# Kernel tuning notes

Hardware: AMD Instinct MI355X
Metric: run time of the kernel (lower is better)

The kernel has to match this reference:

```python
import jax, jax.numpy as jnp
import numpy as np

QC = 12          # effective quantum channels (quantum_channels//4*4)
G = 3            # number of 4-channel quantum groups
DIM = 128
NGROUPS_GN = 8
NUM_LAYER = 1

# PauliZ sign table: wire 0 is the most-significant qubit (PennyLane default.qubit)
_SIGNS = np.array([[1.0 - 2.0 * ((k >> (3 - w)) & 1) for w in range(4)]
                   for k in range(16)], dtype=np.float32)


def _apply_rx(state, phi, w):
    # state: [B,2,2,2,2] complex64; phi: [B]; RX = cos(p/2) I - i sin(p/2) X
    c = jnp.cos(0.5 * phi).astype(jnp.complex64)
    s = (-1j) * jnp.sin(0.5 * phi).astype(jnp.complex64)
    U = jnp.stack([jnp.stack([c, s], -1), jnp.stack([s, c], -1)], -2)  # [B,2,2]
    st = jnp.moveaxis(state, 1 + w, -1)
    st = jnp.einsum('bij,b...j->b...i', U, st)
    return jnp.moveaxis(st, -1, 1 + w)


def _apply_cnot(state, c, t):
    st = jnp.moveaxis(state, (1 + c, 1 + t), (-2, -1))
    st = jnp.concatenate([st[..., 0:1, :], st[..., 1:2, ::-1]], axis=-2)
    return jnp.moveaxis(st, (-2, -1), (1 + c, 1 + t))


def _circuit(x4, theta):
    # AngleEmbedding(RX) + NUM_LAYER x Basic_ansatz; x4: [B,4], theta: [4*NUM_LAYER]
    B = x4.shape[0]
    state = jnp.zeros((B, 2, 2, 2, 2), jnp.complex64).at[:, 0, 0, 0, 0].set(1.0)
    for w in range(4):
        state = _apply_rx(state, x4[:, w], w)
    for l in range(NUM_LAYER):
        th = theta[4 * l:4 * (l + 1)]
        for w in range(4):
            state = _apply_rx(state, jnp.broadcast_to(th[w], (B,)), w)
        for c in range(3):
            state = _apply_cnot(state, c, c + 1)
        state = _apply_cnot(state, 3, 0)
    probs = jnp.abs(state.reshape(B, 16)) ** 2
    return probs @ jnp.asarray(_SIGNS)  # [B,4] PauliZ expvals


def _quantum_block(x_q, qparams):
    # x_q: [B,H,W,QC]; pool spatially, run per-group circuit, broadcast back
    B, H, W, Cq = x_q.shape
    pooled = jnp.mean(x_q, axis=(1, 2)).reshape(B, Cq // 4, 4)
    y = jax.vmap(_circuit, in_axes=(1, 0), out_axes=1)(pooled, qparams)  # [B,G,4]
    y = y.reshape(B, 1, 1, Cq)
    return jnp.broadcast_to(y, (B, H, W, Cq))


def _ws_conv(x, kernel, bias):
    eps = 1e-5  # fp32 branch of WeightStandardizedConv
    mean = jnp.mean(kernel, axis=(0, 1, 2), keepdims=True)
    var = jnp.var(kernel, axis=(0, 1, 2), keepdims=True)
    k = (kernel - mean) / jnp.sqrt(var + eps)
    y = jax.lax.conv_general_dilated(x, k, (1, 1), ((1, 1), (1, 1)),
                                     dimension_numbers=('NHWC', 'HWIO', 'NHWC'))
    return y + bias


def _group_norm(x, scale, bias, groups=NGROUPS_GN, eps=1e-6):
    B, H, W, C = x.shape
    xg = x.reshape(B, H, W, groups, C // groups)
    mu = jnp.mean(xg, axis=(1, 2, 4), keepdims=True)
    var = jnp.var(xg, axis=(1, 2, 4), keepdims=True)
    xn = ((xg - mu) / jnp.sqrt(var + eps)).reshape(B, H, W, C)
    return xn * scale + bias


def setup_inputs() -> dict:
    key = jax.random.key(0)
    ks = jax.random.split(key, 8)
    B, H, W, C, T = 16, 64, 64, DIM, 512
    cc = DIM - QC  # classical conv channels = 116
    return {
        'x': jax.random.normal(ks[0], (B, H, W, C), jnp.float32),
        'time_emb': jax.random.normal(ks[1], (B, T), jnp.float32),
        'qparams': jax.random.uniform(ks[2], (G, 4), jnp.float32),
        'conv0_kernel': jax.random.normal(ks[3], (3, 3, cc, cc), jnp.float32) * 0.05,
        'conv0_bias': jnp.zeros((cc,), jnp.float32),
        'conv1_kernel': jax.random.normal(ks[4], (3, 3, cc, cc), jnp.float32) * 0.05,
        'conv1_bias': jnp.zeros((cc,), jnp.float32),
        'gn0_scale': jnp.ones((C,), jnp.float32),
        'gn0_bias': jnp.zeros((C,), jnp.float32),
        'gn1_scale': jnp.ones((C,), jnp.float32),
        'gn1_bias': jnp.zeros((C,), jnp.float32),
        'time_w': jax.random.normal(ks[5], (T, 2 * DIM), jnp.float32) * 0.02,
        'time_b': jnp.zeros((2 * DIM,), jnp.float32),
    }


def reference(x, time_emb, qparams, conv0_kernel, conv0_bias, conv1_kernel,
              conv1_bias, gn0_scale, gn0_bias, gn1_scale, gn1_bias, time_w, time_b):
    # first quantum + classical branch
    h_q = _quantum_block(x[..., :QC], qparams)
    h_c = _ws_conv(x[..., QC:], conv0_kernel, conv0_bias)
    h = jnp.concatenate([h_q, h_c], axis=-1)
    h = _group_norm(h, gn0_scale, gn0_bias)
    # FiLM conditioning from time embedding
    t = jax.nn.swish(time_emb) @ time_w + time_b  # [B, 2*DIM]
    scale, shift = jnp.split(t[:, None, None, :], 2, axis=-1)
    h = jax.nn.swish(h * (1 + scale) + shift)
    # second quantum + classical branch
    h_q2 = _quantum_block(h[..., :QC], qparams)
    h_c2 = _ws_conv(h[..., QC:], conv1_kernel, conv1_bias)
    h2 = jnp.concatenate([h_q2, h_c2], axis=-1)
    h2 = jax.nn.swish(_group_norm(h2, gn1_scale, gn1_bias))
    return x + h2
```

## Files before the change

kernel.cpp:

```cpp
#include <hip/hip_runtime.h>
#include <math.h>

#define BATCH 16
#define NPX 4096
#define CDIM 128
#define CC 116
#define KTAPS 1044

using u16 = unsigned short;
typedef __attribute__((ext_vector_type(8))) short short8;
typedef __attribute__((ext_vector_type(16))) float f32x16;

__device__ __forceinline__ float swishf(float z) {
    return z / (1.f + __expf(-z));
}
__device__ __forceinline__ float bf2f(u16 u) {
    union { unsigned int i; float f; } v; v.i = ((unsigned int)u) << 16; return v.f;
}
__device__ __forceinline__ u16 f2bf(float f) {
    union { float f; unsigned int i; } v; v.f = f;
    unsigned int r = v.i + 0x7fffu + ((v.i >> 16) & 1u);
    return (u16)(r >> 16);
}

__global__ void k_init(float* __restrict__ p) {
    int i = blockIdx.x * 256 + threadIdx.x;
    if (i < 8384) p[i] = 0.f;
}

__global__ void k_pool(const float* __restrict__ x, float* __restrict__ pooled) {
    int b = blockIdx.x;
    int tid = threadIdx.x;
    float s[12];
#pragma unroll
    for (int c = 0; c < 12; ++c) s[c] = 0.f;
    const float* xb = x + (size_t)b * NPX * CDIM;
    for (int px = tid; px < NPX; px += 256) {
        const float4* p = (const float4*)(xb + (size_t)px * CDIM);
        float4 v0 = p[0], v1 = p[1], v2 = p[2];
        s[0] += v0.x; s[1] += v0.y; s[2] += v0.z; s[3] += v0.w;
        s[4] += v1.x; s[5] += v1.y; s[6] += v1.z; s[7] += v1.w;
        s[8] += v2.x; s[9] += v2.y; s[10] += v2.z; s[11] += v2.w;
    }
    __shared__ float red[12][256];
#pragma unroll
    for (int c = 0; c < 12; ++c) red[c][tid] = s[c];
    __syncthreads();
    for (int st = 128; st > 0; st >>= 1) {
        if (tid < st) {
#pragma unroll
            for (int c = 0; c < 12; ++c) red[c][tid] += red[c][tid + st];
        }
        __syncthreads();
    }
    if (tid < 12) pooled[b * 12 + tid] = red[tid][0] * (1.f / 4096.f);
}

__device__ void run_circuit(const float* ang, const float* th, float* z) {
    float ar[16], ai[16];
#pragma unroll
    for (int k = 0; k < 16; ++k) { ar[k] = 0.f; ai[k] = 0.f; }
    ar[0] = 1.f;
#pragma unroll
    for (int pass = 0; pass < 2; ++pass) {
        const float* a = pass ? th : ang;
#pragma unroll
        for (int w = 0; w < 4; ++w) {
            float half = 0.5f * a[w];
            float cth = cosf(half), sth = sinf(half);
            int m = 1 << (3 - w);
#pragma unroll
            for (int k = 0; k < 16; ++k) {
                if (k & m) continue;
                int k2 = k | m;
                float r0 = ar[k], i0 = ai[k], r1 = ar[k2], i1 = ai[k2];
                ar[k]  = cth * r0 + sth * i1;
                ai[k]  = cth * i0 - sth * r1;
                ar[k2] = sth * i0 + cth * r1;
                ai[k2] = -sth * r0 + cth * i1;
            }
        }
    }
#pragma unroll
    for (int e = 0; e < 4; ++e) {
        const int cwi[4] = {0, 1, 2, 3};
        const int twi[4] = {1, 2, 3, 0};
        int mc = 1 << (3 - cwi[e]), mt = 1 << (3 - twi[e]);
#pragma unroll
        for (int k = 0; k < 16; ++k) {
            if ((k & mc) && !(k & mt)) {
                int k2 = k | mt;
                float tr = ar[k]; ar[k] = ar[k2]; ar[k2] = tr;
                float ti = ai[k]; ai[k] = ai[k2]; ai[k2] = ti;
            }
        }
    }
    float zz[4] = {0.f, 0.f, 0.f, 0.f};
#pragma unroll
    for (int k = 0; k < 16; ++k) {
        float p = ar[k] * ar[k] + ai[k] * ai[k];
#pragma unroll
        for (int w = 0; w < 4; ++w) zz[w] += ((k >> (3 - w)) & 1) ? -p : p;
    }
#pragma unroll
    for (int w = 0; w < 4; ++w) z[w] = zz[w];
}

__global__ void k_circ1(const float* __restrict__ pooled, const float* __restrict__ qp,
                        float* __restrict__ y1) {
    int tid = threadIdx.x;
    if (tid >= 48) return;
    int b = tid / 3, g = tid % 3;
    float z[4];
    run_circuit(pooled + b * 12 + g * 4, qp + g * 4, z);
#pragma unroll
    for (int w = 0; w < 4; ++w) y1[b * 12 + g * 4 + w] = z[w];
}

__global__ void k_time(const float* __restrict__ te, const float* __restrict__ W,
                       const float* __restrict__ tb, float* __restrict__ t) {
    int b = blockIdx.x, tid = threadIdx.x;
    __shared__ float se[512];
    for (int k = tid; k < 512; k += 256) {
        float z = te[b * 512 + k];
        se[k] = swishf(z);
    }
    __syncthreads();
    float acc = tb[tid];
    for (int k = 0; k < 512; ++k) acc += se[k] * W[k * 256 + tid];
    t[b * 256 + tid] = acc;
}

__global__ void k_wstd(const float* __restrict__ K0, const float* __restrict__ K1,
                       u16* __restrict__ kqp0, u16* __restrict__ kqp1) {
    const float* K = blockIdx.y ? K1 : K0;
    u16* kqp = blockIdx.y ? kqp1 : kqp0;
    int o = blockIdx.x;
    int tid = threadIdx.x;
    __shared__ float rs[256], rss[256];
    __shared__ float mb[2];
    float s = 0.f, ss = 0.f;
    if (o < CC) {
        for (int idx = tid; idx < KTAPS; idx += 256) {
            float v = K[(size_t)idx * CC + o];
            s += v; ss += v * v;
        }
    }
    rs[tid] = s; rss[tid] = ss;
    __syncthreads();
    for (int st = 128; st > 0; st >>= 1) {
        if (tid < st) { rs[tid] += rs[tid + st]; rss[tid] += rss[tid + st]; }
        __syncthreads();
    }
    if (tid == 0) {
        float m = rs[0] * (1.f / KTAPS);
        float var = rss[0] * (1.f / KTAPS) - m * m;
        mb[0] = m;
        mb[1] = rsqrtf(var + 1e-5f);
    }
    __syncthreads();
    float m = mb[0], inv = mb[1];
    for (int idx = tid; idx < 1152; idx += 256) {
        int tap = idx >> 7, ic = idx & 127;
        float v = 0.f;
        if (o < CC && ic < CC) v = (K[((size_t)tap * CC + ic) * CC + o] - m) * inv;
        int step = tap * 8 + (ic >> 4);
        int lane2 = ((ic >> 3) & 1) * 32 + (o & 31);
        int j = ic & 7;
        kqp[(size_t)(step * 4 + (o >> 5)) * 512 + lane2 * 8 + j] = f2bf(v);
    }
}

template <int MODE>
__launch_bounds__(256)
__global__ void k_conv(const void* __restrict__ inp, const float* __restrict__ Acoef,
                       const float* __restrict__ Bcoef, const u16* __restrict__ kqp,
                       const float* __restrict__ bias, u16* __restrict__ outp,
                       float* __restrict__ csum) {
    __shared__ u16 As[4 * 64 * 128];
    const int hb = blockIdx.x;
    const int hp = ((hb & 7) << 2) | (hb >> 3);
    const int h0 = hp * 2;
    const int b = blockIdx.y;
    const int tid = threadIdx.x, lane = tid & 63, wid = tid >> 6;
    const int wm = wid & 1, wn = wid >> 1;

    const u16* bp = kqp + ((size_t)(wn * 2) << 9) + ((size_t)lane << 3);
    short8 breg[6][2];
#pragma unroll
    for (int s = 0; s < 6; ++s) {
        breg[s][0] = *(const short8*)(bp + ((size_t)s << 11));
        breg[s][1] = *(const short8*)(bp + ((size_t)s << 11) + 512);
    }

    const int pp = tid >> 2, ck = tid & 3;
    const int swz = (pp & 15) << 4;
    char* asb = (char*)As;

    float ca[32], cb[32];
    if (MODE == 1) {
        const float* ap = Acoef + b * 128 + 12 + ck * 32;
        const float* bpc = Bcoef + b * 128 + 12 + ck * 32;
        if (ck < 3) {
#pragma unroll
            for (int j = 0; j < 8; ++j) {
                *(float4*)&ca[j * 4] = ((const float4*)ap)[j];
                *(float4*)&cb[j * 4] = ((const float4*)bpc)[j];
            }
        } else {
#pragma unroll
            for (int j = 0; j < 5; ++j) {
                *(float4*)&ca[j * 4] = ((const float4*)ap)[j];
                *(float4*)&cb[j * 4] = ((const float4*)bpc)[j];
            }
        }
    }

#pragma unroll
    for (int r = 0; r < 4; ++r) {
        const int hi = h0 + r - 1;
        const bool valid = (hi >= 0 && hi < 64);
        u16 t[32];
        if (valid) {
            const size_t px = (size_t)((b * 64 + hi) * 64 + pp);
            if (MODE == 0) {
                const float* s = (const float*)inp + px * 128 + 12 + ck * 32;
                if (ck < 3) {
                    float v[32];
#pragma unroll
                    for (int j = 0; j < 8; ++j) *(float4*)&v[j * 4] = ((const float4*)s)[j];
#pragma unroll
                    for (int e = 0; e < 32; ++e) t[e] = f2bf(v[e]);
                } else {
                    float v[20];
#pragma unroll
                    for (int j = 0; j < 5; ++j) *(float4*)&v[j * 4] = ((const float4*)s)[j];
#pragma unroll
                    for (int e = 0; e < 20; ++e) t[e] = f2bf(v[e]);
#pragma unroll
                    for (int e = 20; e < 32; ++e) t[e] = 0;
                }
            } else {
                const u16* s = (const u16*)inp + px * 128 + ck * 32;
                if (ck < 3) {
                    short8 v[4];
#pragma unroll
                    for (int k = 0; k < 4; ++k) v[k] = ((const short8*)s)[k];
#pragma unroll
                    for (int e = 0; e < 32; ++e) {
                        float f = bf2f((u16)v[e >> 3][e & 7]);
                        t[e] = f2bf(swishf(f * ca[e] + cb[e]));
                    }
                } else {
                    short8 v[3];
#pragma unroll
                    for (int k = 0; k < 3; ++k) v[k] = ((const short8*)s)[k];
#pragma unroll
                    for (int e = 0; e < 20; ++e) {
                        float f = bf2f((u16)v[e >> 3][e & 7]);
                        t[e] = f2bf(swishf(f * ca[e] + cb[e]));
                    }
#pragma unroll
                    for (int e = 20; e < 32; ++e) t[e] = 0;
                }
            }
        } else {
#pragma unroll
            for (int e = 0; e < 32; ++e) t[e] = 0;
        }
        char* rowb = asb + (r * 64 + pp) * 256;
#pragma unroll
        for (int k = 0; k < 4; ++k)
            *(short8*)(rowb + (((ck * 64 + k * 16)) ^ swz)) = *(const short8*)&t[k * 8];
    }

    const int l31 = lane & 31;
    const int chpart = (lane >> 5) << 4;
    int rowoff[3], swzv[3];
#pragma unroll
    for (int q = 0; q < 3; ++q) {
        int ppx = l31 + q - 1;
        int ppc = ppx < 0 ? 0 : ppx;
        rowoff[q] = ppc << 7;
        swzv[q] = (ppc & 15) << 4;
    }
    int rowoff1[3], swzv1[3];
#pragma unroll
    for (int q = 0; q < 3; ++q) {
        int ppx = 32 + l31 + q - 1;
        int ppc = ppx > 63 ? 63 : ppx;
        rowoff1[q] = ppc << 7;
        swzv1[q] = (ppc & 15) << 4;
    }
    const bool edge_lo = (l31 == 0);
    const bool edge_hi = (l31 == 31);
    const short8 zero8 = {0, 0, 0, 0, 0, 0, 0, 0};
    const u16* aw = As + wm * 8192;

    __syncthreads();

    f32x16 acc[2][2];
#pragma unroll
    for (int mf = 0; mf < 2; ++mf)
#pragma unroll
        for (int nf = 0; nf < 2; ++nf)
#pragma unroll
            for (int r = 0; r < 16; ++r) acc[mf][nf][r] = 0.f;

    short8 afrag[2][2];
    afrag[0][0] = *(const short8*)&aw[rowoff[0] + ((chpart ^ swzv[0]) >> 1)];
    afrag[0][1] = *(const short8*)&aw[rowoff1[0] + ((chpart ^ swzv1[0]) >> 1)];

#pragma unroll
    for (int s = 0; s < 72; ++s) {
        const int tap = s >> 3;
        const int p = tap / 3, q = tap % 3;
        const int slotB = s % 6;
        const int cur = s & 1, nxt = cur ^ 1;
        if (s + 1 < 72) {
            const int t2 = (s + 1) >> 3;
            const int p2 = t2 / 3, q2 = t2 % 3;
            const int cb2 = ((s + 1) & 7) << 5;
            afrag[nxt][0] = *(const short8*)&aw[p2 * 8192 + rowoff[q2]
                             + (((cb2 + chpart) ^ swzv[q2]) >> 1)];
            afrag[nxt][1] = *(const short8*)&aw[p2 * 8192 + rowoff1[q2]
                             + (((cb2 + chpart) ^ swzv1[q2]) >> 1)];
        }
        short8 a0 = afrag[cur][0], a1 = afrag[cur][1];
        if (q == 0) a0 = edge_lo ? zero8 : a0;
        if (q == 2) a1 = edge_hi ? zero8 : a1;
        acc[0][0] = __builtin_amdgcn_mfma_f32_32x32x16_bf16(a0, breg[slotB][0], acc[0][0], 0, 0, 0);
        acc[0][1] = __builtin_amdgcn_mfma_f32_32x32x16_bf16(a0, breg[slotB][1], acc[0][1], 0, 0, 0);
        acc[1][0] = __builtin_amdgcn_mfma_f32_32x32x16_bf16(a1, breg[slotB][0], acc[1][0], 0, 0, 0);
        acc[1][1] = __builtin_amdgcn_mfma_f32_32x32x16_bf16(a1, breg[slotB][1], acc[1][1], 0, 0, 0);
        if (s + 6 < 72) {
            breg[slotB][0] = *(const short8*)(bp + ((size_t)(s + 6) << 11));
            breg[slotB][1] = *(const short8*)(bp + ((size_t)(s + 6) << 11) + 512);
        }
    }

    float bv[2], cs[2], cq[2];
#pragma unroll
    for (int nf = 0; nf < 2; ++nf) {
        int oc = wn * 64 + nf * 32 + l31;
        bv[nf] = (oc < CC) ? bias[oc] : 0.f;
        cs[nf] = 0.f; cq[nf] = 0.f;
    }
    const int rbase = (lane >> 5) * 4;
    size_t obase = (size_t)(b * 4096 + (h0 + wm) * 64) * 128;
#pragma unroll
    for (int mf = 0; mf < 2; ++mf)
#pragma unroll
        for (int nf = 0; nf < 2; ++nf) {
            int oc = wn * 64 + nf * 32 + l31;
#pragma unroll
            for (int r = 0; r < 16; ++r) {
                int row = (r & 3) + ((r >> 2) << 3) + rbase;
                int px = mf * 32 + row;
                float v = acc[mf][nf][r] + bv[nf];
                outp[obase + (size_t)px * 128 + oc] = f2bf(v);
                cs[nf] += v;
                cq[nf] += v * v;
            }
        }
#pragma unroll
    for (int nf = 0; nf < 2; ++nf) {
        cs[nf] += __shfl_xor(cs[nf], 32);
        cq[nf] += __shfl_xor(cq[nf], 32);
        if (lane < 32) {
            int oc = wn * 64 + nf * 32 + l31;
            atomicAdd(&csum[(b * 128 + oc) * 2], cs[nf]);
            atomicAdd(&csum[(b * 128 + oc) * 2 + 1], cq[nf]);
        }
    }
}

__global__ void k_mid0(const float* __restrict__ csum, const float* __restrict__ y1,
                       const float* __restrict__ t, const float* __restrict__ gs,
                       const float* __restrict__ gb, const float* __restrict__ qp,
                       float* __restrict__ A, float* __restrict__ Bc,
                       float* __restrict__ y2) {
    __shared__ float sst[128][2];
    int tid = threadIdx.x;
    if (tid < 128) {
        int b = tid >> 3, g = tid & 7;
        float S = 0.f, SS = 0.f;
#pragma unroll
        for (int e = 0; e < 16; ++e) {
            int orig = g * 16 + e;
            if (orig >= 12) {
                int cc = orig - 12;
                S += csum[(b * 128 + cc) * 2];
                SS += csum[(b * 128 + cc) * 2 + 1];
            }
        }
        if (g == 0) {
#pragma unroll
            for (int c = 0; c < 12; ++c) {
                float v = y1[b * 12 + c];
                S += 4096.f * v;
                SS += 4096.f * v * v;
            }
        }
        float mu = S * (1.f / 65536.f);
        float var = SS * (1.f / 65536.f) - mu * mu;
        sst[tid][0] = mu;
        sst[tid][1] = rsqrtf(var + 1e-6f);
    }
    __syncthreads();
    for (int i = tid; i < 2048; i += 256) {
        int b = i >> 7, c = i & 127, g = c >> 4;
        float mu = sst[b * 8 + g][0], isd = sst[b * 8 + g][1];
        float sc = t[b * 256 + c], sh = t[b * 256 + 128 + c];
        float a = isd * gs[c];
        float bb = gb[c] - mu * a;
        A[i] = a * (1.f + sc);
        Bc[i] = bb * (1.f + sc) + sh;
    }
    if (tid < 48) {
        int b = tid / 3, gq = tid % 3;
        float pin[4], z[4];
        float mu = sst[b * 8][0], isd = sst[b * 8][1];
#pragma unroll
        for (int w = 0; w < 4; ++w) {
            int c = gq * 4 + w;
            float a = isd * gs[c];
            float bb = gb[c] - mu * a;
            float sc = t[b * 256 + c], sh = t[b * 256 + 128 + c];
            float v = y1[b * 12 + c];
            pin[w] = swishf(v * (a * (1.f + sc)) + (bb * (1.f + sc) + sh));
        }
        run_circuit(pin, qp + gq * 4, z);
#pragma unroll
        for (int w = 0; w < 4; ++w) y2[b * 12 + gq * 4 + w] = z[w];
    }
}

__global__ void k_mid1(const float* __restrict__ csum, const float* __restrict__ y2,
                       const float* __restrict__ gs, const float* __restrict__ gb,
                       float* __restrict__ A2, float* __restrict__ B2,
                       float* __restrict__ oq) {
    __shared__ float sst[128][2];
    int tid = threadIdx.x;
    if (tid < 128) {
        int b = tid >> 3, g = tid & 7;
        float S = 0.f, SS = 0.f;
#pragma unroll
        for (int e = 0; e < 16; ++e) {
            int orig = g * 16 + e;
            if (orig >= 12) {
                int cc = orig - 12;
                S += csum[(b * 128 + cc) * 2];
                SS += csum[(b * 128 + cc) * 2 + 1];
            }
        }
        if (g == 0) {
#pragma unroll
            for (int c = 0; c < 12; ++c) {
                float v = y2[b * 12 + c];
                S += 4096.f * v;
                SS += 4096.f * v * v;
            }
        }
        float mu = S * (1.f / 65536.f);
        float var = SS * (1.f / 65536.f) - mu * mu;
        sst[tid][0] = mu;
        sst[tid][1] = rsqrtf(var + 1e-6f);
    }
    __syncthreads();
    for (int i = tid; i < 2048; i += 256) {
        int b = i >> 7, c = i & 127, g = c >> 4;
        float mu = sst[b * 8 + g][0], isd = sst[b * 8 + g][1];
        float a = isd * gs[c];
        A2[i] = a;
        B2[i] = gb[c] - mu * a;
    }
    if (tid < 192) {
        int b = tid / 12, c = tid % 12;
        float mu = sst[b * 8][0], isd = sst[b * 8][1];
        float a = isd * gs[c];
        float bb = gb[c] - mu * a;
        oq[b * 12 + c] = swishf(y2[b * 12 + c] * a + bb);
    }
}

__global__ void k_final(const float* __restrict__ x, const u16* __restrict__ co,
                        const float* __restrict__ A2, const float* __restrict__ B2,
                        const float* __restrict__ oq, float* __restrict__ outp) {
    const int t = blockIdx.x, b = blockIdx.y;
    const int seg = t >> 6, hraw = t & 63;
    const int h = ((hraw & 7) << 3) | (hraw >> 3);
    const int tid = threadIdx.x;
    const size_t px = (size_t)(b * 64 + h) * 64 + seg * 8 + (tid >> 5);
    const int c4 = tid & 31, c = c4 * 4;
    float4 xv = *(const float4*)(x + px * CDIM + c);
    float4 r;
    if (c4 < 3) {
        const float* q = oq + b * 12 + c;
        r.x = xv.x + q[0]; r.y = xv.y + q[1]; r.z = xv.z + q[2]; r.w = xv.w + q[3];
    } else {
        int cc = c - 12;
        const u16* hp = co + px * 128 + cc;
        float4 a = *(const float4*)(A2 + b * 128 + c);
        float4 bb = *(const float4*)(B2 + b * 128 + c);
        r.x = xv.x + swishf(bf2f(hp[0]) * a.x + bb.x);
        r.y = xv.y + swishf(bf2f(hp[1]) * a.y + bb.y);
        r.z = xv.z + swishf(bf2f(hp[2]) * a.z + bb.z);
        r.w = xv.w + swishf(bf2f(hp[3]) * a.w + bb.w);
    }
    *(float4*)(outp + px * CDIM + c) = r;
}

extern "C" void kernel_launch(void* const* d_in, const int* in_sizes, int n_in,
                              void* d_out, int out_size, void* d_ws, size_t ws_size,
                              hipStream_t stream) {
    const float* x        = (const float*)d_in[0];
    const float* time_emb = (const float*)d_in[1];
    const float* qparams  = (const float*)d_in[2];
    const float* c0k      = (const float*)d_in[3];
    const float* c0b      = (const float*)d_in[4];
    const float* c1k      = (const float*)d_in[5];
    const float* c1b      = (const float*)d_in[6];
    const float* g0s      = (const float*)d_in[7];
    const float* g0b      = (const float*)d_in[8];
    const float* g1s      = (const float*)d_in[9];
    const float* g1b      = (const float*)d_in[10];
    const float* tw       = (const float*)d_in[11];
    const float* tb       = (const float*)d_in[12];
    float* outp = (float*)d_out;
    float* ws = (float*)d_ws;

    size_t o = 0;
    auto alloc = [&](size_t n) { size_t r = o; o += (n + 15) & ~(size_t)15; return r; };
    float* zbase  = ws + alloc(8384);
    float* pooled = zbase;
    float* csum0  = zbase + 192;
    float* csum1  = zbase + 192 + 4096;
    float* y1     = ws + alloc(192);
    float* y2     = ws + alloc(192);
    float* t      = ws + alloc(4096);
    float* A      = ws + alloc(2048);
    float* Bc     = ws + alloc(2048);
    float* A2     = ws + alloc(2048);
    float* B2     = ws + alloc(2048);
    float* oq     = ws + alloc(192);
    u16* kqp0     = (u16*)(ws + alloc(73728));
    u16* kqp1     = (u16*)(ws + alloc(73728));
    u16* convA    = (u16*)(ws + alloc(4194304));
    u16* convB    = (u16*)(ws + alloc(4194304));

    k_init<<<33, 256, 0, stream>>>(zbase);
    k_pool<<<16, 256, 0, stream>>>(x, pooled);
    k_time<<<16, 256, 0, stream>>>(time_emb, tw, tb, t);
    k_wstd<<<dim3(128, 2), 256, 0, stream>>>(c0k, c1k, kqp0, kqp1);
    k_circ1<<<1, 64, 0, stream>>>(pooled, qparams, y1);

    dim3 cgrid(32, 16);
    k_conv<0><<<cgrid, 256, 0, stream>>>(x, nullptr, nullptr, kqp0, c0b, convA, csum0);
    k_mid0<<<1, 256, 0, stream>>>(csum0, y1, t, g0s, g0b, qparams, A, Bc, y2);

    k_conv<1><<<cgrid, 256, 0, stream>>>(convA, A, Bc, kqp1, c1b, convB, csum1);
    k_mid1<<<1, 256, 0, stream>>>(csum1, y2, g1s, g1b, A2, B2, oq);
    k_final<<<dim3(512, 16), 256, 0, stream>>>(x, convB, A2, B2, oq, outp);
}
```

Measured before the change: 135.9 us.

## Split conv LDS staging to overlap MFMA on first rows with loading the rest

The conv kernel now issues all four input-row global loads up front, writes only rows 0-1 to LDS, and starts MFMA on taps using those rows (the first 24 steps). Rows 2-3 are converted and stored only after that, behind a second barrier. It also uses the hardware packed bf16 convert instruction, raises MFMA priority with s_setprio, shrinks the B-register prefetch ring from 6 to 3 slots, and sets launch_bounds to 2 blocks per SM. Holding the raw rows in registers increases register pressure, and the shallower B prefetch may expose more load latency.

Result: faster. 129.9 us (-4.4%).

```diff
diff --git a/kernel.cpp b/kernel.cpp
--- a/kernel.cpp
+++ b/kernel.cpp
@@ -21,6 +21,11 @@
     union { float f; unsigned int i; } v; v.f = f;
     unsigned int r = v.i + 0x7fffu + ((v.i >> 16) & 1u);
     return (u16)(r >> 16);
+}
+__device__ __forceinline__ unsigned cvtpk(float a, float b) {
+    unsigned r;
+    asm("v_cvt_pk_bf16_f32 %0, %1, %2" : "=v"(r) : "v"(a), "v"(b));
+    return r;
 }
 
 __global__ void k_init(float* __restrict__ p) {
@@ -172,7 +177,7 @@
 }
 
 template <int MODE>
-__launch_bounds__(256)
+__launch_bounds__(256, 2)
 __global__ void k_conv(const void* __restrict__ inp, const float* __restrict__ Acoef,
                        const float* __restrict__ Bcoef, const u16* __restrict__ kqp,
                        const float* __restrict__ bias, u16* __restrict__ outp,
@@ -184,95 +189,85 @@
     const int b = blockIdx.y;
     const int tid = threadIdx.x, lane = tid & 63, wid = tid >> 6;
     const int wm = wid & 1, wn = wid >> 1;
-
-    const u16* bp = kqp + ((size_t)(wn * 2) << 9) + ((size_t)lane << 3);
-    short8 breg[6][2];
-#pragma unroll
-    for (int s = 0; s < 6; ++s) {
-        breg[s][0] = *(const short8*)(bp + ((size_t)s << 11));
-        breg[s][1] = *(const short8*)(bp + ((size_t)s << 11) + 512);
-    }
-
     const int pp = tid >> 2, ck = tid & 3;
     const int swz = (pp & 15) << 4;
     char* asb = (char*)As;
+
+    float fr0[32], fr1[32], fr2[32], fr3[32];
+    short8 sr0[4], sr1[4], sr2[4], sr3[4];
+    bool val[4];
+
+#define LOADROW(r, fv, sv)  do { \
+    const int hi_ = h0 + (r) - 1; \
+    val[r] = (hi_ >= 0 && hi_ < 64); \
+    if (val[r]) { \
+        const size_t px_ = (size_t)((b * 64 + hi_) * 64 + pp); \
+        if (MODE == 0) { \
+            const float* sp_ = (const float*)inp + px_ * 128 + 12 + ck * 32; \
+            if (ck < 3) { \
+                _Pragma("unroll") for (int j = 0; j < 8; ++j) *(float4*)&fv[j * 4] = ((const float4*)sp_)[j]; \
+            } else { \
+                _Pragma("unroll") for (int j = 0; j < 5; ++j) *(float4*)&fv[j * 4] = ((const float4*)sp_)[j]; \
+                _Pragma("unroll") for (int e = 20; e < 32; ++e) fv[e] = 0.f; \
+            } \
+        } else { \
+            const u16* sp_ = (const u16*)inp + px_ * 128 + ck * 32; \
+            _Pragma("unroll") for (int k = 0; k < 4; ++k) sv[k] = ((const short8*)sp_)[k]; \
+        } \
+    } \
+} while (0)
+
+    LOADROW(0, fr0, sr0);
+    LOADROW(1, fr1, sr1);
+    LOADROW(2, fr2, sr2);
+    LOADROW(3, fr3, sr3);
 
     float ca[32], cb[32];
     if (MODE == 1) {
         const float* ap = Acoef + b * 128 + 12 + ck * 32;
         const float* bpc = Bcoef + b * 128 + 12 + ck * 32;
-        if (ck < 3) {
-#pragma unroll
-            for (int j = 0; j < 8; ++j) {
+        const int nj = (ck < 3) ? 8 : 5;
+#pragma unroll
+        for (int j = 0; j < 8; ++j)
+            if (j < nj) {
                 *(float4*)&ca[j * 4] = ((const float4*)ap)[j];
                 *(float4*)&cb[j * 4] = ((const float4*)bpc)[j];
             }
-        } else {
-#pragma unroll
-            for (int j = 0; j < 5; ++j) {
-                *(float4*)&ca[j * 4] = ((const float4*)ap)[j];
-                *(float4*)&cb[j * 4] = ((const float4*)bpc)[j];
-            }
-        }
-    }
-
-#pragma unroll
-    for (int r = 0; r < 4; ++r) {
-        const int hi = h0 + r - 1;
-        const bool valid = (hi >= 0 && hi < 64);
-        u16 t[32];
-        if (valid) {
-            const size_t px = (size_t)((b * 64 + hi) * 64 + pp);
-            if (MODE == 0) {
-                const float* s = (const float*)inp + px * 128 + 12 + ck * 32;
-                if (ck < 3) {
-                    float v[32];
-#pragma unroll
-                    for (int j = 0; j < 8; ++j) *(float4*)&v[j * 4] = ((const float4*)s)[j];
-#pragma unroll
-                    for (int e = 0; e < 32; ++e) t[e] = f2bf(v[e]);
-                } else {
-                    float v[20];
-#pragma unroll
-                    for (int j = 0; j < 5; ++j) *(float4*)&v[j * 4] = ((const float4*)s)[j];
-#pragma unroll
-                    for (int e = 0; e < 20; ++e) t[e] = f2bf(v[e]);
-#pragma unroll
-                    for (int e = 20; e < 32; ++e) t[e] = 0;
-                }
-            } else {
-                const u16* s = (const u16*)inp + px * 128 + ck * 32;
-                if (ck < 3) {
-                    short8 v[4];
-#pragma unroll
-                    for (int k = 0; k < 4; ++k) v[k] = ((const short8*)s)[k];
-#pragma unroll
-                    for (int e = 0; e < 32; ++e) {
-                        float f = bf2f((u16)v[e >> 3][e & 7]);
-                        t[e] = f2bf(swishf(f * ca[e] + cb[e]));
-                    }
-                } else {
-                    short8 v[3];
-#pragma unroll
-                    for (int k = 0; k < 3; ++k) v[k] = ((const short8*)s)[k];
-#pragma unroll
-                    for (int e = 0; e < 20; ++e) {
-                        float f = bf2f((u16)v[e >> 3][e & 7]);
-                        t[e] = f2bf(swishf(f * ca[e] + cb[e]));
-                    }
-#pragma unroll
-                    for (int e = 20; e < 32; ++e) t[e] = 0;
-                }
-            }
-        } else {
-#pragma unroll
-            for (int e = 0; e < 32; ++e) t[e] = 0;
-        }
-        char* rowb = asb + (r * 64 + pp) * 256;
-#pragma unroll
-        for (int k = 0; k < 4; ++k)
-            *(short8*)(rowb + (((ck * 64 + k * 16)) ^ swz)) = *(const short8*)&t[k * 8];
-    }
+        if (ck == 3) {
+#pragma unroll
+            for (int e = 20; e < 32; ++e) { ca[e] = 0.f; cb[e] = 0.f; }
+        }
+    }
+
+    const u16* bp = kqp + ((size_t)(wn * 2) << 9) + ((size_t)lane << 3);
+    short8 breg[3][2];
+#pragma unroll
+    for (int s = 0; s < 3; ++s) {
+        breg[s][0] = *(const short8*)(bp + ((size_t)s << 11));
+        breg[s][1] = *(const short8*)(bp + ((size_t)s << 11) + 512);
+    }
+
+#define WRITEROW(r, fv, sv) do { \
+    unsigned pk_[16]; \
+    if (val[r]) { \
+        if (MODE == 0) { \
+            _Pragma("unroll") for (int e = 0; e < 16; ++e) pk_[e] = cvtpk(fv[2 * e], fv[2 * e + 1]); \
+        } else { \
+            float g_[32]; \
+            _Pragma("unroll") for (int e = 0; e < 32; ++e) { \
+                float f_ = bf2f((u16)sv[e >> 3][e & 7]); \
+                float w_ = swishf(f_ * ca[e] + cb[e]); \
+                g_[e] = (e >= 20 && ck == 3) ? 0.f : w_; \
+            } \
+            _Pragma("unroll") for (int e = 0; e < 16; ++e) pk_[e] = cvtpk(g_[2 * e], g_[2 * e + 1]); \
+        } \
+    } else { \
+        _Pragma("unroll") for (int e = 0; e < 16; ++e) pk_[e] = 0u; \
+    } \
+    char* rowb_ = asb + ((r) * 64 + pp) * 256; \
+    _Pragma("unroll") for (int k = 0; k < 4; ++k) \
+        *(short8*)(rowb_ + ((ck * 64 + k * 16) ^ swz)) = *(const short8*)&pk_[k * 4]; \
+} while (0)
 
     const int l31 = lane & 31;
     const int chpart = (lane >> 5) << 4;
@@ -297,6 +292,8 @@
     const short8 zero8 = {0, 0, 0, 0, 0, 0, 0, 0};
     const u16* aw = As + wm * 8192;
 
+    WRITEROW(0, fr0, sr0);
+    WRITEROW(1, fr1, sr1);
     __syncthreads();
 
     f32x16 acc[2][2];
@@ -307,36 +304,49 @@
 #pragma unroll
             for (int r = 0; r < 16; ++r) acc[mf][nf][r] = 0.f;
 
+#define AREAD(dst, s) do { \
+    const int tap_ = (s) >> 3, p2_ = tap_ / 3, q2_ = tap_ % 3; \
+    const int cb2_ = ((s) & 7) << 5; \
+    dst[0] = *(const short8*)&aw[p2_ * 8192 + rowoff[q2_] + (((cb2_ + chpart) ^ swzv[q2_]) >> 1)]; \
+    dst[1] = *(const short8*)&aw[p2_ * 8192 + rowoff1[q2_] + (((cb2_ + chpart) ^ swzv1[q2_]) >> 1)]; \
+} while (0)
+
+#define DOSTEP(s, cur, nxt, lim) do { \
+    const int slotB_ = (s) % 3; \
+    if ((s) + 1 < (lim)) AREAD(afrag[nxt], (s) + 1); \
+    const int q_ = ((s) >> 3) % 3; \
+    short8 a0_ = afrag[cur][0], a1_ = afrag[cur][1]; \
+    if (q_ == 0) a0_ = edge_lo ? zero8 : a0_; \
+    if (q_ == 2) a1_ = edge_hi ? zero8 : a1_; \
+    __builtin_amdgcn_s_setprio(1); \
+    acc[0][0] = __builtin_amdgcn_mfma_f32_32x32x16_bf16(a0_, breg[slotB_][0], acc[0][0], 0, 0, 0); \
+    acc[0][1] = __builtin_amdgcn_mfma_f32_32x32x16_bf16(a0_, breg[slotB_][1], acc[0][1], 0, 0, 0); \
+    acc[1][0] = __builtin_amdgcn_mfma_f32_32x32x16_bf16(a1_, breg[slotB_][0], acc[1][0], 0, 0, 0); \
+    acc[1][1] = __builtin_amdgcn_mfma_f32_32x32x16_bf16(a1_, breg[slotB_][1], acc[1][1], 0, 0, 0); \
+    __builtin_amdgcn_s_setprio(0); \
+    if ((s) + 3 < 72) { \
+        breg[slotB_][0] = *(const short8*)(bp + ((size_t)((s) + 3) << 11)); \
+        breg[slotB_][1] = *(const short8*)(bp + ((size_t)((s) + 3) << 11) + 512); \
+    } \
+} while (0)
+
     short8 afrag[2][2];
-    afrag[0][0] = *(const short8*)&aw[rowoff[0] + ((chpart ^ swzv[0]) >> 1)];
-    afrag[0][1] = *(const short8*)&aw[rowoff1[0] + ((chpart ^ swzv1[0]) >> 1)];
-
-#pragma unroll
-    for (int s = 0; s < 72; ++s) {
-        const int tap = s >> 3;
-        const int p = tap / 3, q = tap % 3;
-        const int slotB = s % 6;
+    AREAD(afrag[0], 0);
+#pragma unroll
+    for (int s = 0; s < 24; ++s) {
         const int cur = s & 1, nxt = cur ^ 1;
-        if (s + 1 < 72) {
-            const int t2 = (s + 1) >> 3;
-            const int p2 = t2 / 3, q2 = t2 % 3;
-            const int cb2 = ((s + 1) & 7) << 5;
-            afrag[nxt][0] = *(const short8*)&aw[p2 * 8192 + rowoff[q2]
-                             + (((cb2 + chpart) ^ swzv[q2]) >> 1)];
-            afrag[nxt][1] = *(const short8*)&aw[p2 * 8192 + rowoff1[q2]
-                             + (((cb2 + chpart) ^ swzv1[q2]) >> 1)];
-        }
-        short8 a0 = afrag[cur][0], a1 = afrag[cur][1];
-        if (q == 0) a0 = edge_lo ? zero8 : a0;
-        if (q == 2) a1 = edge_hi ? zero8 : a1;
-        acc[0][0] = __builtin_amdgcn_mfma_f32_32x32x16_bf16(a0, breg[slotB][0], acc[0][0], 0, 0, 0);
-        acc[0][1] = __builtin_amdgcn_mfma_f32_32x32x16_bf16(a0, breg[slotB][1], acc[0][1], 0, 0, 0);
-        acc[1][0] = __builtin_amdgcn_mfma_f32_32x32x16_bf16(a1, breg[slotB][0], acc[1][0], 0, 0, 0);
-        acc[1][1] = __builtin_amdgcn_mfma_f32_32x32x16_bf16(a1, breg[slotB][1], acc[1][1], 0, 0, 0);
-        if (s + 6 < 72) {
-            breg[slotB][0] = *(const short8*)(bp + ((size_t)(s + 6) << 11));
-            breg[slotB][1] = *(const short8*)(bp + ((size_t)(s + 6) << 11) + 512);
-        }
+        DOSTEP(s, cur, nxt, 24);
+    }
+
+    WRITEROW(2, fr2, sr2);
+    WRITEROW(3, fr3, sr3);
+    __syncthreads();
+
+    AREAD(afrag[0], 24);
+#pragma unroll
+    for (int s = 24; s < 72; ++s) {
+        const int cur = (s - 24) & 1, nxt = cur ^ 1;
+        DOSTEP(s, cur, nxt, 72);
     }
 
     float bv[2], cs[2], cq[2];
@@ -358,7 +368,7 @@
                 int row = (r & 3) + ((r >> 2) << 3) + rbase;
                 int px = mf * 32 + row;
                 float v = acc[mf][nf][r] + bv[nf];
-                outp[obase + (size_t)px * 128 + oc] = f2bf(v);
+                outp[obase + (size_t)px * 128 + oc] = (u16)cvtpk(v, v);
                 cs[nf] += v;
                 cq[nf] += v * v;
             }
@@ -373,6 +383,10 @@
             atomicAdd(&csum[(b * 128 + oc) * 2 + 1], cq[nf]);
         }
     }
+#undef LOADROW
+#undef WRITEROW
+#undef AREAD
+#undef DOSTEP
 }
 
 __global__ void k_mid0(const float* __restrict__ csum, const float* __restrict__ y1,
```
